# Performance work log

Measured on AMD Instinct MI355X. Metric: run time of the kernel, lower is better.

## Reference

```python
import jax, jax.numpy as jnp
import numpy as np

NC = 16          # tess_size
HID = 128
DIM = 8
N_BATCH = 400000


def make_basis(nC):
    # Constraint matrix L for 1D CPA velocity field v_c(x)=a_c*x+b_c on [0,1]:
    #   continuity at internal knots x_k=(k+1)/nC, and zero boundary v(0)=v(1)=0.
    # Basis B = SVD null space of L (cpab library, basis='svd').
    L = np.zeros((nC + 1, 2 * nC), dtype=np.float64)
    for k in range(nC - 1):
        xk = (k + 1) / nC
        L[k, 2 * k] = xk
        L[k, 2 * k + 1] = 1.0
        L[k, 2 * k + 2] = -xk
        L[k, 2 * k + 3] = -1.0
    L[nC - 1, 1] = 1.0                     # v(0)=0 -> b_0 = 0
    L[nC, 2 * nC - 2] = 1.0                # v(1)=0 -> a_{nC-1}+b_{nC-1}=0
    L[nC, 2 * nC - 1] = 1.0
    _, _, vh = np.linalg.svd(L)
    B = vh[L.shape[0]:].T                  # (2*nC, nC-1)
    return B.astype(np.float32)


def cpab_integrate(x, A, nC):
    """Closed-form CPAB integration of dx/dt = a_c x + b_c for t in [0,1],
    with cell hopping; also accumulates log of the space gradient
    d(phi)/dx = exp(sum_c a_c * tau_c).  x: (N,), A: (N, nC, 2)."""
    eps = 1e-8
    aC, bC = A[:, :, 0], A[:, :, 1]
    c0 = jnp.clip(jnp.floor(x * nC).astype(jnp.int32), 0, nC - 1)
    carry0 = (x, jnp.ones_like(x), c0, jnp.zeros_like(x),
              jnp.zeros(x.shape, dtype=bool))

    def step(carry, _):
        xx, t, c, logg, done = carry
        a = jnp.take_along_axis(aC, c[:, None], axis=1)[:, 0]
        b = jnp.take_along_axis(bC, c[:, None], axis=1)[:, 0]
        v = a * xx + b
        small_a = jnp.abs(a) < eps
        a_safe = jnp.where(small_a, 1.0, a)
        eat = jnp.exp(a * t)
        # solution of the affine ODE within the current cell for remaining time t
        psi = jnp.where(small_a, xx + b * t,
                        eat * xx + (b / a_safe) * (eat - 1.0))
        left = c.astype(x.dtype) / nC
        right = (c + 1).astype(x.dtype) / nC
        inside = (psi >= left) & (psi <= right)
        xc = jnp.where(v >= 0, right, left)          # boundary being approached
        v_safe = jnp.where(jnp.abs(v) < eps, 1.0, v)
        b_safe = jnp.where(jnp.abs(b) < eps, 1.0, b)
        ratio = jnp.maximum((a * xc + b) / v_safe, eps)
        thit = jnp.where(small_a, (xc - xx) / b_safe,
                         jnp.log(ratio) / a_safe)     # time to hit boundary
        tau = jnp.where(inside, t, thit)              # time spent in this cell
        new_done = done | inside
        xx2 = jnp.where(done, xx, jnp.where(inside, psi, xc))
        logg2 = jnp.where(done, logg, logg + a * tau)
        t2 = jnp.where(new_done, t, t - thit)
        c2 = jnp.where(new_done, c,
                       jnp.clip(c + jnp.where(v >= 0, 1, -1), 0, nC - 1))
        return (xx2, t2, c2, logg2, new_done), None

    (xf, _, _, loggf, _), _ = jax.lax.scan(step, carry0, None, length=nC + 2)
    return xf, loggf


def setup_inputs() -> dict:
    key = jax.random.key(0)
    n, dim, hidden, nC = N_BATCH, DIM, HID, NC
    d = nC - 1
    lower = dim // 2
    upper = dim - lower
    ks = jax.random.split(key, 6)
    s = 0.3
    x = jax.random.uniform(ks[0], (n, dim), dtype=jnp.float32)
    W0 = jax.random.normal(ks[1], (lower, hidden), jnp.float32) * s
    b0 = jnp.zeros((hidden,), jnp.float32)
    W1 = jax.random.normal(ks[2], (hidden, hidden), jnp.float32) * s / np.sqrt(hidden)
    b1 = jnp.zeros((hidden,), jnp.float32)
    W2 = jax.random.normal(ks[3], (hidden, hidden), jnp.float32) * s / np.sqrt(hidden)
    b2 = jnp.zeros((hidden,), jnp.float32)
    W3 = jax.random.normal(ks[4], (hidden, hidden), jnp.float32) * s / np.sqrt(hidden)
    b3 = jnp.zeros((hidden,), jnp.float32)
    Wo = jax.random.normal(ks[5], (hidden, d * upper), jnp.float32) * s / np.sqrt(hidden)
    bo = jnp.zeros((d * upper,), jnp.float32)
    B = jnp.asarray(make_basis(nC))
    return dict(x=x, W0=W0, b0=b0, W1=W1, b1=b1, W2=W2, b2=b2, W3=W3, b3=b3,
                Wo=Wo, bo=bo, B=B)


def reference(x, W0, b0, W1, b1, W2, b2, W3, b3, Wo, bo, B):
    n, dim = x.shape
    lower = dim // 2
    upper = dim - lower
    nC = B.shape[0] // 2
    d = B.shape[1]
    x1, x2 = x[:, :lower], x[:, lower:]
    h = x1 @ W0 + b0
    h = jnp.maximum(h @ W1 + b1, 0.0)
    h = jnp.maximum(h @ W2 + b2, 0.0)
    h = jnp.maximum(h @ W3 + b3, 0.0)
    theta = (h @ Wo + bo).reshape(-1, d)          # (n*upper, d)
    A = (theta @ B.T).reshape(-1, nC, 2)          # per-point CPA field
    z2, logg = cpab_integrate(x2.reshape(-1), A, nC)
    z = jnp.concatenate([x1, z2.reshape(n, upper)], axis=1)
    log_dz_dx = jnp.concatenate(
        [jnp.zeros((n, lower), x.dtype), logg.reshape(n, upper)], axis=1)
    return z, log_dz_dx
```

## Files before the change

### kernel.cpp

```cpp
#include <hip/hip_runtime.h>
#include <stdint.h>

#define N_BATCH 400000
#define BM 64
#define NBLK (N_BATCH / BM)

typedef __bf16 bf16x8 __attribute__((ext_vector_type(8)));
typedef float  f32x4  __attribute__((ext_vector_type(4)));

__device__ __forceinline__ uint16_t f2bf(float f) {
    union { float f; uint32_t u; } x; x.f = f;
    uint32_t u = x.u;
    uint32_t r = (u + 0x7FFFu + ((u >> 16) & 1u)) >> 16;
    return (uint16_t)r;
}
__device__ __forceinline__ float bf2f(uint16_t h) {
    union { uint32_t u; float f; } x; x.u = ((uint32_t)h) << 16;
    return x.f;
}
__device__ __forceinline__ int swzi(int row, int chan) {
    return row * 128 + (chan ^ ((row & 7) << 3));
}

__global__ void pack_kernel(const float* __restrict__ W1, const float* __restrict__ W2,
                            const float* __restrict__ W3, const float* __restrict__ Wo,
                            const float* __restrict__ bo, const float* __restrict__ B,
                            uint16_t* __restrict__ pwh, uint16_t* __restrict__ pwl,
                            float* __restrict__ bo2) {
    if (blockIdx.x == 256) {
        int t = threadIdx.x;
        if (t < 128) {
            int dim = t >> 5, j = t & 31;
            float s = 0.f;
            for (int d = 0; d < 15; ++d) s += bo[dim * 15 + d] * B[j * 15 + d];
            bo2[t] = s;
        }
        return;
    }
    int gid = blockIdx.x * 256 + threadIdx.x;
    int L    = gid >> 14;
    int r    = gid & 16383;
    int j    = r & 7;
    int lane = (r >> 3) & 63;
    int nf   = (r >> 9) & 7;
    int ks   = r >> 12;
    int k = ks * 32 + (lane >> 4) * 8 + j;
    int n = nf * 16 + (lane & 15);
    float v;
    if (L == 3) {
        int dim = n >> 5, jj = n & 31;
        float s = 0.f;
        for (int d = 0; d < 15; ++d) s += Wo[k * 60 + dim * 15 + d] * B[jj * 15 + d];
        v = s;
    } else {
        const float* W = (L == 0) ? W1 : (L == 1) ? W2 : W3;
        v = W[k * 128 + n];
    }
    uint16_t h = f2bf(v);
    pwh[gid] = h;
    pwl[gid] = f2bf(v - bf2f(h));
}

__global__ void __launch_bounds__(256) cpab_kernel(
    const float* __restrict__ x, const float* __restrict__ W0,
    const float* __restrict__ b0, const float* __restrict__ b1,
    const float* __restrict__ b2, const float* __restrict__ b3,
    const __bf16* __restrict__ pwh, const __bf16* __restrict__ pwl,
    const float* __restrict__ bo2,
    float* __restrict__ outz, float* __restrict__ outl)
{
    __shared__ __align__(16) uint8_t smem[32 * 1024];
    __bf16* Hh = (__bf16*)smem;
    __bf16* Hl = Hh + BM * 128;
    float*  Af = (float*)smem;

    const int tid  = threadIdx.x;
    const int blk  = blockIdx.x;
    const int lane = tid & 63;
    const int wid  = tid >> 6;
    const int ml   = lane & 15;
    const int hl   = lane >> 4;
    const float* xrow = x + (size_t)blk * (BM * 8);

    {
        int j0 = (tid & 15) * 8;
        float wc[4][8], bc[8];
        #pragma unroll
        for (int k = 0; k < 4; ++k) {
            float4 lo = *(const float4*)&W0[k * 128 + j0];
            float4 hi = *(const float4*)&W0[k * 128 + j0 + 4];
            wc[k][0]=lo.x; wc[k][1]=lo.y; wc[k][2]=lo.z; wc[k][3]=lo.w;
            wc[k][4]=hi.x; wc[k][5]=hi.y; wc[k][6]=hi.z; wc[k][7]=hi.w;
        }
        {
            float4 lo = *(const float4*)&b0[j0];
            float4 hi = *(const float4*)&b0[j0 + 4];
            bc[0]=lo.x; bc[1]=lo.y; bc[2]=lo.z; bc[3]=lo.w;
            bc[4]=hi.x; bc[5]=hi.y; bc[6]=hi.z; bc[7]=hi.w;
        }
        #pragma unroll
        for (int i = 0; i < 4; ++i) {
            int row = (tid >> 4) + i * 16;
            float4 xv = *(const float4*)&xrow[row * 8];
            bf16x8 hv, lv;
            #pragma unroll
            for (int jj = 0; jj < 8; ++jj) {
                float v = bc[jj] + xv.x*wc[0][jj] + xv.y*wc[1][jj] + xv.z*wc[2][jj] + xv.w*wc[3][jj];
                __bf16 h = (__bf16)v;
                hv[jj] = h;
                lv[jj] = (__bf16)(v - (float)h);
            }
            int idx = swzi(row, j0);
            *(bf16x8*)&Hh[idx] = hv;
            *(bf16x8*)&Hl[idx] = lv;
        }
    }
    __syncthreads();

    auto gemm = [&](const __bf16* wh, const __bf16* wl,
                    const float* bias, bool relu, bool final_f32) {
        float bv0 = bias[wid * 32 + 0  + ml];
        float bv1 = bias[wid * 32 + 16 + ml];

        f32x4 acc[4][2];
        #pragma unroll
        for (int m = 0; m < 4; ++m)
            #pragma unroll
            for (int n = 0; n < 2; ++n)
                acc[m][n] = (f32x4){0.f, 0.f, 0.f, 0.f};

        __builtin_amdgcn_s_setprio(1);
        #pragma unroll
        for (int ks = 0; ks < 4; ++ks) {
            bf16x8 ah[4], al[4];
            #pragma unroll
            for (int m = 0; m < 4; ++m) {
                int idx = swzi(m * 16 + ml, ks * 32 + hl * 8);
                ah[m] = *(const bf16x8*)&Hh[idx];
                al[m] = *(const bf16x8*)&Hl[idx];
            }
            #pragma unroll
            for (int n = 0; n < 2; ++n) {
                int nf = wid * 2 + n;
                int widx = ((ks * 8 + nf) * 64 + lane) * 8;
                bf16x8 bh = *(const bf16x8*)&wh[widx];
                bf16x8 bl = *(const bf16x8*)&wl[widx];
                #pragma unroll
                for (int m = 0; m < 4; ++m) {
                    acc[m][n] = __builtin_amdgcn_mfma_f32_16x16x32_bf16(al[m], bl, acc[m][n], 0, 0, 0);
                    acc[m][n] = __builtin_amdgcn_mfma_f32_16x16x32_bf16(al[m], bh, acc[m][n], 0, 0, 0);
                    acc[m][n] = __builtin_amdgcn_mfma_f32_16x16x32_bf16(ah[m], bl, acc[m][n], 0, 0, 0);
                    acc[m][n] = __builtin_amdgcn_mfma_f32_16x16x32_bf16(ah[m], bh, acc[m][n], 0, 0, 0);
                }
            }
        }
        __builtin_amdgcn_s_setprio(0);
        __syncthreads();
        #pragma unroll
        for (int n = 0; n < 2; ++n) {
            int col = wid * 32 + n * 16 + ml;
            float bv = n ? bv1 : bv0;
            #pragma unroll
            for (int m = 0; m < 4; ++m) {
                #pragma unroll
                for (int r = 0; r < 4; ++r) {
                    int row = m * 16 + hl * 4 + r;
                    float v = acc[m][n][r] + bv;
                    if (relu) v = fmaxf(v, 0.f);
                    int idx = swzi(row, col);
                    if (final_f32) {
                        Af[idx] = v;
                    } else {
                        __bf16 h = (__bf16)v;
                        Hh[idx] = h;
                        Hl[idx] = (__bf16)(v - (float)h);
                    }
                }
            }
        }
        __syncthreads();
    };

    gemm(pwh + 0*16384, pwl + 0*16384, b1,  true,  false);
    gemm(pwh + 1*16384, pwl + 1*16384, b2,  true,  false);
    gemm(pwh + 2*16384, pwl + 2*16384, b3,  true,  false);
    gemm(pwh + 3*16384, pwl + 3*16384, bo2, false, true);

    {
        int row = tid >> 2, dim = tid & 3;
        float xx = xrow[row * 8 + 4 + dim];
        int c = (int)floorf(xx * 16.f);
        c = min(max(c, 0), 15);
        float t = 1.f, logg = 0.f;
        bool done = false;
        #pragma unroll 1
        for (int it = 0; it < 18; ++it) {
            if (__all(done)) break;
            int ci = swzi(row, (dim << 5) + 2 * c);
            float2 ab = *(const float2*)&Af[ci];
            float a = ab.x, b = ab.y;
            float v = a * xx + b;
            bool small_a = fabsf(a) < 1e-8f;
            float a_safe = small_a ? 1.f : a;
            float eat = expf(a * t);
            float psi = small_a ? (xx + b * t) : (eat * xx + (b / a_safe) * (eat - 1.f));
            float left  = (float)c * 0.0625f;
            float right = (float)(c + 1) * 0.0625f;
            bool inside = (psi >= left) && (psi <= right);
            float xc = (v >= 0.f) ? right : left;
            float v_safe = (fabsf(v) < 1e-8f) ? 1.f : v;
            float b_safe = (fabsf(b) < 1e-8f) ? 1.f : b;
            float ratio = fmaxf((a * xc + b) / v_safe, 1e-8f);
            float thit = small_a ? ((xc - xx) / b_safe) : (logf(ratio) / a_safe);
            float tau = inside ? t : thit;
            bool new_done = done || inside;
            if (!done) {
                xx = inside ? psi : xc;
                logg = logg + a * tau;
            }
            if (!new_done) {
                t = t - thit;
                c = min(max(c + ((v >= 0.f) ? 1 : -1), 0), 15);
            }
            done = new_done;
        }
        size_t grow = (size_t)blk * BM + row;
        outz[grow * 8 + 4 + dim] = xx;
        outl[grow * 8 + 4 + dim] = logg;
        outz[grow * 8 + dim]     = xrow[row * 8 + dim];
        outl[grow * 8 + dim]     = 0.f;
    }
}

extern "C" void kernel_launch(void* const* d_in, const int* in_sizes, int n_in,
                              void* d_out, int out_size, void* d_ws, size_t ws_size,
                              hipStream_t stream) {
    const float* x  = (const float*)d_in[0];
    const float* W0 = (const float*)d_in[1];
    const float* b0 = (const float*)d_in[2];
    const float* W1 = (const float*)d_in[3];
    const float* b1 = (const float*)d_in[4];
    const float* W2 = (const float*)d_in[5];
    const float* b2 = (const float*)d_in[6];
    const float* W3 = (const float*)d_in[7];
    const float* b3 = (const float*)d_in[8];
    const float* Wo = (const float*)d_in[9];
    const float* bo = (const float*)d_in[10];
    const float* B  = (const float*)d_in[11];

    uint16_t* pwh = (uint16_t*)d_ws;
    uint16_t* pwl = pwh + 4 * 16384;
    float*    bo2 = (float*)(pwl + 4 * 16384);
    float*    outz = (float*)d_out;
    float*    outl = outz + (size_t)N_BATCH * 8;

    hipLaunchKernelGGL(pack_kernel, dim3(257), dim3(256), 0, stream,
                       W1, W2, W3, Wo, bo, B, pwh, pwl, bo2);
    hipLaunchKernelGGL(cpab_kernel, dim3(NBLK), dim3(256), 0, stream,
                       x, W0, b0, b1, b2, b3,
                       (const __bf16*)pwh, (const __bf16*)pwl, bo2, outz, outl);
}
```

Measured before the change: 176.6 us.

## Give each wavefront its own 32-row tile to drop block-wide barriers

```diff
diff --git a/kernel.cpp b/kernel.cpp
--- a/kernel.cpp
+++ b/kernel.cpp
@@ -2,7 +2,9 @@
 #include <stdint.h>
 
 #define N_BATCH 400000
-#define BM 64
+#define BMW 32
+#define WPB 2
+#define BM (BMW * WPB)
 #define NBLK (N_BATCH / BM)
 
 typedef __bf16 bf16x8 __attribute__((ext_vector_type(8)));
@@ -61,7 +63,7 @@
     pwl[gid] = f2bf(v - bf2f(h));
 }
 
-__global__ void __launch_bounds__(256) cpab_kernel(
+__global__ void __launch_bounds__(128, 2) cpab_kernel(
     const float* __restrict__ x, const float* __restrict__ W0,
     const float* __restrict__ b0, const float* __restrict__ b1,
     const float* __restrict__ b2, const float* __restrict__ b3,
@@ -69,21 +71,23 @@
     const float* __restrict__ bo2,
     float* __restrict__ outz, float* __restrict__ outl)
 {
-    __shared__ __align__(16) uint8_t smem[32 * 1024];
-    __bf16* Hh = (__bf16*)smem;
-    __bf16* Hl = Hh + BM * 128;
-    float*  Af = (float*)smem;
+    __shared__ __align__(16) uint8_t smem[WPB * 16 * 1024];
 
     const int tid  = threadIdx.x;
-    const int blk  = blockIdx.x;
     const int lane = tid & 63;
     const int wid  = tid >> 6;
     const int ml   = lane & 15;
     const int hl   = lane >> 4;
-    const float* xrow = x + (size_t)blk * (BM * 8);
+
+    __bf16* Hh = (__bf16*)(smem + wid * 16384);
+    __bf16* Hl = Hh + BMW * 128;
+    float*  Af = (float*)(smem + wid * 16384);
+
+    const size_t rowbase = (size_t)blockIdx.x * BM + (size_t)wid * BMW;
+    const float* xrow = x + rowbase * 8;
 
     {
-        int j0 = (tid & 15) * 8;
+        int j0 = ml * 8;
         float wc[4][8], bc[8];
         #pragma unroll
         for (int k = 0; k < 4; ++k) {
@@ -99,8 +103,8 @@
             bc[4]=hi.x; bc[5]=hi.y; bc[6]=hi.z; bc[7]=hi.w;
         }
         #pragma unroll
-        for (int i = 0; i < 4; ++i) {
-            int row = (tid >> 4) + i * 16;
+        for (int i = 0; i < 8; ++i) {
+            int row = hl + i * 4;
             float4 xv = *(const float4*)&xrow[row * 8];
             bf16x8 hv, lv;
             #pragma unroll
@@ -115,38 +119,33 @@
             *(bf16x8*)&Hl[idx] = lv;
         }
     }
-    __syncthreads();
 
     auto gemm = [&](const __bf16* wh, const __bf16* wl,
                     const float* bias, bool relu, bool final_f32) {
-        float bv0 = bias[wid * 32 + 0  + ml];
-        float bv1 = bias[wid * 32 + 16 + ml];
-
-        f32x4 acc[4][2];
-        #pragma unroll
-        for (int m = 0; m < 4; ++m)
-            #pragma unroll
-            for (int n = 0; n < 2; ++n)
+        f32x4 acc[2][8];
+        #pragma unroll
+        for (int m = 0; m < 2; ++m)
+            #pragma unroll
+            for (int n = 0; n < 8; ++n)
                 acc[m][n] = (f32x4){0.f, 0.f, 0.f, 0.f};
 
         __builtin_amdgcn_s_setprio(1);
         #pragma unroll
         for (int ks = 0; ks < 4; ++ks) {
-            bf16x8 ah[4], al[4];
-            #pragma unroll
-            for (int m = 0; m < 4; ++m) {
+            bf16x8 ah[2], al[2];
+            #pragma unroll
+            for (int m = 0; m < 2; ++m) {
                 int idx = swzi(m * 16 + ml, ks * 32 + hl * 8);
                 ah[m] = *(const bf16x8*)&Hh[idx];
                 al[m] = *(const bf16x8*)&Hl[idx];
             }
             #pragma unroll
-            for (int n = 0; n < 2; ++n) {
-                int nf = wid * 2 + n;
-                int widx = ((ks * 8 + nf) * 64 + lane) * 8;
+            for (int n = 0; n < 8; ++n) {
+                int widx = ((ks * 8 + n) * 64 + lane) * 8;
                 bf16x8 bh = *(const bf16x8*)&wh[widx];
                 bf16x8 bl = *(const bf16x8*)&wl[widx];
                 #pragma unroll
-                for (int m = 0; m < 4; ++m) {
+                for (int m = 0; m < 2; ++m) {
                     acc[m][n] = __builtin_amdgcn_mfma_f32_16x16x32_bf16(al[m], bl, acc[m][n], 0, 0, 0);
                     acc[m][n] = __builtin_amdgcn_mfma_f32_16x16x32_bf16(al[m], bh, acc[m][n], 0, 0, 0);
                     acc[m][n] = __builtin_amdgcn_mfma_f32_16x16x32_bf16(ah[m], bl, acc[m][n], 0, 0, 0);
@@ -155,13 +154,12 @@
             }
         }
         __builtin_amdgcn_s_setprio(0);
-        __syncthreads();
-        #pragma unroll
-        for (int n = 0; n < 2; ++n) {
-            int col = wid * 32 + n * 16 + ml;
-            float bv = n ? bv1 : bv0;
-            #pragma unroll
-            for (int m = 0; m < 4; ++m) {
+        #pragma unroll
+        for (int n = 0; n < 8; ++n) {
+            int col = n * 16 + ml;
+            float bv = bias[col];
+            #pragma unroll
+            for (int m = 0; m < 2; ++m) {
                 #pragma unroll
                 for (int r = 0; r < 4; ++r) {
                     int row = m * 16 + hl * 4 + r;
@@ -178,7 +176,6 @@
                 }
             }
         }
-        __syncthreads();
     };
 
     gemm(pwh + 0*16384, pwl + 0*16384, b1,  true,  false);
@@ -186,8 +183,10 @@
     gemm(pwh + 2*16384, pwl + 2*16384, b3,  true,  false);
     gemm(pwh + 3*16384, pwl + 3*16384, bo2, false, true);
 
-    {
-        int row = tid >> 2, dim = tid & 3;
+    #pragma unroll 1
+    for (int q = 0; q < 2; ++q) {
+        int e   = lane + q * 64;
+        int row = e >> 2, dim = e & 3;
         float xx = xrow[row * 8 + 4 + dim];
         int c = (int)floorf(xx * 16.f);
         c = min(max(c, 0), 15);
@@ -224,7 +223,7 @@
             }
             done = new_done;
         }
-        size_t grow = (size_t)blk * BM + row;
+        size_t grow = rowbase + row;
         outz[grow * 8 + 4 + dim] = xx;
         outl[grow * 8 + 4 + dim] = logg;
         outz[grow * 8 + dim]     = xrow[row * 8 + dim];
@@ -256,7 +255,7 @@
 
     hipLaunchKernelGGL(pack_kernel, dim3(257), dim3(256), 0, stream,
                        W1, W2, W3, Wo, bo, B, pwh, pwl, bo2);
-    hipLaunchKernelGGL(cpab_kernel, dim3(NBLK), dim3(256), 0, stream,
+    hipLaunchKernelGGL(cpab_kernel, dim3(NBLK), dim3(128), 0, stream,
                        x, W0, b0, b1, b2, b3,
                        (const __bf16*)pwh, (const __bf16*)pwl, bo2, outz, outl);
 }
```

After: 230.3 us. 1.3x slower.
